# Optimization experiments

Hardware: AMD Instinct MI355X
Metric: run time of the kernel (lower is better)

## Reference

```python
import jax, jax.numpy as jnp
import numpy as np

N, F_IN, F_OUT, K = 4096, 32, 32, 2
NEG_SLOPE = 0.2
MASK_VAL = -9e15


def _sparse_mat(kv, km, density=0.01):
    vals = jax.random.normal(kv, (N, N), dtype=jnp.float32)
    mask = jax.random.uniform(km, (N, N)) < density
    return vals * mask


def setup_inputs() -> dict:
    key = jax.random.key(0)
    ks = jax.random.split(key, 12)
    x = jax.random.normal(ks[0], (N, F_IN), dtype=jnp.float32)
    Ld = _sparse_mat(ks[1], ks[2])
    Lu = _sparse_mat(ks[3], ks[4])
    P = jax.random.normal(ks[5], (N, N), dtype=jnp.float32) / np.sqrt(N)
    W1 = jax.random.normal(ks[6], (K, F_IN, F_OUT), dtype=jnp.float32) * 0.1
    W2 = jax.random.normal(ks[7], (K, F_IN, F_OUT), dtype=jnp.float32) * 0.1
    W0 = jax.random.normal(ks[8], (F_IN, F_OUT), dtype=jnp.float32) * 0.1
    att1 = jax.random.normal(ks[9], (2 * F_OUT * K, 1), dtype=jnp.float32) * 0.1
    att2 = jax.random.normal(ks[10], (2 * F_OUT * K, 1), dtype=jnp.float32) * 0.1
    return {"x": x, "Ld": Ld, "Lu": Lu, "P": P, "W1": W1, "W2": W2,
            "W0": W0, "att1": att1, "att2": att2}


def _branch(x, L, W, att):
    # W: [K, F_in, F_out]; precompute x @ W[k] for all k -> [K, N, F_out]
    Kk, _, Fo = W.shape
    xw = jnp.einsum('nf,kfo->kno', x, W)
    # torch.cat([x@W[k]], dim=1) == transpose+reshape of xw
    xcat = jnp.transpose(xw, (1, 0, 2)).reshape(x.shape[0], Kk * Fo)
    d = Fo * Kk
    e = xcat @ att[:d] + (xcat @ att[d:]).T            # [N, N]
    e = jax.nn.leaky_relu(e, negative_slope=NEG_SLOPE)
    e = jnp.where(L != 0, e, MASK_VAL)
    alpha = jax.nn.softmax(e, axis=1)                   # row softmax, no dropout (eval)
    z = alpha @ xw[0]
    a = alpha
    for k in range(1, Kk):
        a = a @ L
        z = z + a @ xw[k]
    return z


def reference(x, Ld, Lu, P, W1, W2, W0, att1, att2):
    z1 = _branch(x, Ld, W1, att1)
    z2 = _branch(x, Lu, W2, att2)
    x0 = P @ (x @ W0)
    return z1 + z2 + x0
```

## Files before the change

### kernel.cpp

```cpp
#include <hip/hip_runtime.h>
#include <hip/hip_bf16.h>

#define NN 4096
#define CAP 128
#define KS 8
#define PGB 512

typedef __attribute__((ext_vector_type(8))) short bf16x8;
typedef __attribute__((ext_vector_type(4))) float f32x4;

__device__ __forceinline__ float lrelu(float v) { return v >= 0.f ? v : 0.2f * v; }

__device__ __forceinline__ ushort f2bu(float f) {
    unsigned u = __float_as_uint(f);
    return (ushort)((u + 0x7FFFu + ((u >> 16) & 1u)) >> 16);
}

__global__ __launch_bounds__(256) void k_prep(
    const float* __restrict__ x,
    const float* __restrict__ W1, const float* __restrict__ W2,
    const float* __restrict__ W0,
    const float* __restrict__ att1, const float* __restrict__ att2,
    float* __restrict__ xwA1, float* __restrict__ xwB1,
    float* __restrict__ xwA2, float* __restrict__ xwB2,
    float* __restrict__ a1, float* __restrict__ b1,
    float* __restrict__ a2, float* __restrict__ b2,
    __hip_bfloat16* __restrict__ Bt)
{
    __shared__ float wl[5120];
    __shared__ float xs[256];
    const int t = threadIdx.x;
    for (int i = t; i < 2048; i += 256) { wl[i] = W1[i]; wl[2048 + i] = W2[i]; }
    for (int i = t; i < 1024; i += 256) wl[4096 + i] = W0[i];
    const int rowBase = blockIdx.x * 8;
    xs[t] = x[rowBase * 32 + t];
    __syncthreads();

    const int o = t & 31, r = t >> 5;
    const int row = rowBase + r;
    const float* xr = &xs[r * 32];
    float vA1 = 0.f, vB1 = 0.f, vA2 = 0.f, vB2 = 0.f, v0 = 0.f;
#pragma unroll
    for (int f = 0; f < 32; ++f) {
        const float xv = xr[f];
        vA1 += xv * wl[f * 32 + o];
        vB1 += xv * wl[1024 + f * 32 + o];
        vA2 += xv * wl[2048 + f * 32 + o];
        vB2 += xv * wl[3072 + f * 32 + o];
        v0  += xv * wl[4096 + f * 32 + o];
    }
    xwA1[row * 32 + o] = vA1;
    xwB1[row * 32 + o] = vB1;
    xwA2[row * 32 + o] = vA2;
    xwB2[row * 32 + o] = vB2;
    ((ushort*)Bt)[(size_t)o * NN + row] = f2bu(v0);

    float pa1 = vA1 * att1[o]      + vB1 * att1[32 + o];
    float pb1 = vA1 * att1[64 + o] + vB1 * att1[96 + o];
    float pa2 = vA2 * att2[o]      + vB2 * att2[32 + o];
    float pb2 = vA2 * att2[64 + o] + vB2 * att2[96 + o];
#pragma unroll
    for (int m = 1; m <= 16; m <<= 1) {
        pa1 += __shfl_xor(pa1, m); pb1 += __shfl_xor(pb1, m);
        pa2 += __shfl_xor(pa2, m); pb2 += __shfl_xor(pb2, m);
    }
    if (o == 0) { a1[row] = pa1; b1[row] = pb1; a2[row] = pa2; b2[row] = pb2; }
}

__global__ __launch_bounds__(256) void k_fused(
    const float* __restrict__ Ld, const float* __restrict__ Lu,
    const float* __restrict__ xwB1, const float* __restrict__ xwB2,
    const float* __restrict__ xwA1, const float* __restrict__ xwA2,
    const float* __restrict__ a1, const float* __restrict__ b1,
    const float* __restrict__ a2, const float* __restrict__ b2,
    int2* __restrict__ csrv, int* __restrict__ cntArr,
    float* __restrict__ u1, float* __restrict__ u2,
    const float* __restrict__ P, const ushort* __restrict__ Bt,
    float* __restrict__ partial)
{
    __shared__ int   sidx[CAP];
    __shared__ float sval[CAP];
    __shared__ int   wcnt[16];
    __shared__ float red[256];
    __shared__ float rpart[8];

    const int bid = blockIdx.x;
    const int t = threadIdx.x;
    const int lane = t & 63, w = t >> 6;

    if (bid < PGB) {
        const int gw = bid * 4 + w;
        const int mt = gw & 255;
        const int ks = gw >> 8;
        const int m0 = mt * 16;
        const int r  = lane & 15;
        const int kq = lane >> 4;

        const float*  pa  = P  + (size_t)(m0 + r) * NN + ks * 512 + kq * 8;
        const ushort* pb0 = Bt + (size_t)r        * NN + ks * 512 + kq * 8;
        const ushort* pb1 = Bt + (size_t)(16 + r) * NN + ks * 512 + kq * 8;

        f32x4 acc0 = {0.f, 0.f, 0.f, 0.f};
        f32x4 acc1 = {0.f, 0.f, 0.f, 0.f};

#pragma unroll 4
        for (int kk = 0; kk < 16; ++kk) {
            const float4 a0 = *(const float4*)(pa + kk * 32);
            const float4 a1v = *(const float4*)(pa + kk * 32 + 4);
            const bf16x8 b0 = *(const bf16x8*)(pb0 + kk * 32);
            const bf16x8 b1v = *(const bf16x8*)(pb1 + kk * 32);
            bf16x8 a;
            a[0] = (short)f2bu(a0.x); a[1] = (short)f2bu(a0.y);
            a[2] = (short)f2bu(a0.z); a[3] = (short)f2bu(a0.w);
            a[4] = (short)f2bu(a1v.x); a[5] = (short)f2bu(a1v.y);
            a[6] = (short)f2bu(a1v.z); a[7] = (short)f2bu(a1v.w);
            acc0 = __builtin_amdgcn_mfma_f32_16x16x32_bf16(a, b0, acc0, 0, 0, 0);
            acc1 = __builtin_amdgcn_mfma_f32_16x16x32_bf16(a, b1v, acc1, 0, 0, 0);
        }

        float* out = partial + ((size_t)ks * NN + m0 + kq * 4) * 32;
#pragma unroll
        for (int rr = 0; rr < 4; ++rr) {
            out[rr * 32 + r]      = acc0[rr];
            out[rr * 32 + 16 + r] = acc1[rr];
        }
        return;
    }

    const int sb  = bid - PGB;
    const int br  = sb >> 12;
    const int row = sb & (NN - 1);
    const float* L   = br ? Lu : Ld;
    const float* xwB = br ? xwB2 : xwB1;
    const float* xwA = br ? xwA2 : xwA1;
    const float* aA  = br ? a2 : a1;
    const float* bA  = br ? b2 : b1;
    int2* csrB = csrv + ((size_t)br * NN + row) * CAP;
    float* u   = br ? u2 : u1;

    const float4* L4 = (const float4*)(L + (size_t)row * NN);
    float4 v[4];
#pragma unroll
    for (int it = 0; it < 4; ++it) v[it] = L4[it * 256 + t];

    const unsigned long long lt = (1ull << lane) - 1ull;

    unsigned long long M0[4], M1[4], M2[4], M3[4];
    int tots[4];
#pragma unroll
    for (int it = 0; it < 4; ++it) {
        M0[it] = __ballot(v[it].x != 0.f);
        M1[it] = __ballot(v[it].y != 0.f);
        M2[it] = __ballot(v[it].z != 0.f);
        M3[it] = __ballot(v[it].w != 0.f);
        tots[it] = __popcll(M0[it]) + __popcll(M1[it]) + __popcll(M2[it]) + __popcll(M3[it]);
    }
    if (lane == 0) {
        int4 tv; tv.x = tots[0]; tv.y = tots[1]; tv.z = tots[2]; tv.w = tots[3];
        *(int4*)&wcnt[w * 4] = tv;
    }
    __syncthreads();

    const int4 ca = *(const int4*)&wcnt[0];
    const int4 cb = *(const int4*)&wcnt[4];
    const int4 cc = *(const int4*)&wcnt[8];
    const int4 cd = *(const int4*)&wcnt[12];
    const int cs[16] = {ca.x, ca.y, ca.z, ca.w, cb.x, cb.y, cb.z, cb.w,
                        cc.x, cc.y, cc.z, cc.w, cd.x, cd.y, cd.z, cd.w};
    int total = 0;
#pragma unroll
    for (int k2 = 0; k2 < 16; ++k2) total += cs[k2];
    int base = 0;
#pragma unroll
    for (int k2 = 0; k2 < 16; ++k2) base += (k2 < (w << 2)) ? cs[k2] : 0;

    const int cnt  = min(total, CAP);
    const int cp16 = min((cnt + 15) & ~15, CAP);

#pragma unroll
    for (int it = 0; it < 4; ++it) {
        const float vx = v[it].x, vy = v[it].y, vz = v[it].z, vw = v[it].w;
        const int p0 = __popcll(M0[it]), p1 = __popcll(M1[it]), p2 = __popcll(M2[it]);
        const int c0 = (it * 256 + t) * 4;
        int s;
        s = base + __popcll(M0[it] & lt);
        if (vx != 0.f && s < CAP) { sidx[s] = c0;     sval[s] = vx; }
        s = base + p0 + __popcll(M1[it] & lt);
        if (vy != 0.f && s < CAP) { sidx[s] = c0 + 1; sval[s] = vy; }
        s = base + p0 + p1 + __popcll(M2[it] & lt);
        if (vz != 0.f && s < CAP) { sidx[s] = c0 + 2; sval[s] = vz; }
        s = base + p0 + p1 + p2 + __popcll(M3[it] & lt);
        if (vw != 0.f && s < CAP) { sidx[s] = c0 + 3; sval[s] = vw; }
        base += p0 + p1 + p2 + __popcll(M3[it]);
    }
    if (t >= cnt && t < cp16) { sidx[t] = 0; sval[t] = 0.f; }
    __syncthreads();

    const float ai = aA[row];
    const int myidx = (t < cp16) ? sidx[t] : 0;
    const float e = (t < cnt) ? lrelu(ai + bA[myidx]) : -1e30f;
    float m = e;
#pragma unroll
    for (int mm = 1; mm <= 32; mm <<= 1) m = fmaxf(m, __shfl_xor(m, mm));
    if (lane == 0) rpart[w] = m;
    __syncthreads();
    m = fmaxf(fmaxf(rpart[0], rpart[1]), fmaxf(rpart[2], rpart[3]));
    const float wgt = (t < cnt) ? __expf(e - m) : 0.f;
    float ss = wgt;
#pragma unroll
    for (int mm = 1; mm <= 32; mm <<= 1) ss += __shfl_xor(ss, mm);
    if (lane == 0) rpart[4 + w] = ss;
    __syncthreads();
    const float ssum = rpart[4] + rpart[5] + rpart[6] + rpart[7];
    const float inv = (cnt > 0) ? 1.f / ssum : 0.f;
    if (t < cp16) { int2 eo; eo.x = myidx; eo.y = __float_as_int(wgt * inv); csrB[t] = eo; }
    if (t == 0) cntArr[br * NN + row] = cnt;

    const int o = t & 31, g = t >> 5;
    float acc = 0.f;
    const int nPair = cp16 >> 4;
    if (nPair > 0) {
        float vA0 = sval[g],      vA1 = sval[g + 8];
        float xA0 = xwB[(size_t)sidx[g] * 32 + o];
        float xA1 = xwB[(size_t)sidx[g + 8] * 32 + o];
        for (int j = 1; j < nPair; ++j) {
            const int sB = g + 16 * j;
            const float vB0 = sval[sB],  vB1 = sval[sB + 8];
            const float xB0 = xwB[(size_t)sidx[sB] * 32 + o];
            const float xB1 = xwB[(size_t)sidx[sB + 8] * 32 + o];
            acc += vA0 * xA0 + vA1 * xA1;
            vA0 = vB0; xA0 = xB0; vA1 = vB1; xA1 = xB1;
        }
        acc += vA0 * xA0 + vA1 * xA1;
    }
    red[t] = acc;
    __syncthreads();
    if (t < 32) {
        float tot2 = 0.f;
#pragma unroll
        for (int g2 = 0; g2 < 8; ++g2) tot2 += red[g2 * 32 + t];
        u[(size_t)row * 32 + t] = tot2 + xwA[(size_t)row * 32 + t];
    }
}

__global__ __launch_bounds__(256) void k_accum(
    const int2* __restrict__ csrv, const int* __restrict__ cntArr,
    const float* __restrict__ u1, const float* __restrict__ u2,
    const float* __restrict__ partial, float* __restrict__ outp)
{
    __shared__ int2 sle[4][2 * CAP];
    const int w = threadIdx.x >> 6, lane = threadIdx.x & 63;
    const int row = blockIdx.x * 4 + w;
    const int o = lane & 31, g = lane >> 5;
    int2* se = sle[w];
    float total = 0.f;

    int cp[2];
#pragma unroll
    for (int br = 0; br < 2; ++br) {
        const int cnt = cntArr[br * NN + row];
        cp[br] = min((cnt + 15) & ~15, CAP);
        const int2* ci = csrv + ((size_t)br * NN + row) * CAP;
        if (lane < cp[br])      se[br * CAP + lane]      = ci[lane];
        if (lane + 64 < cp[br]) se[br * CAP + lane + 64] = ci[lane + 64];
    }

#pragma unroll
    for (int br = 0; br < 2; ++br) {
        const float* U = br ? u2 : u1;
        float acc = 0.f;
        const int nb = cp[br] >> 3;
        for (int j = 0; j < nb; ++j) {
            float wv[4], uv[4];
#pragma unroll
            for (int q = 0; q < 4; ++q) {
                const int2 e = se[br * CAP + 8 * j + 2 * q + g];
                wv[q] = __int_as_float(e.y);
                uv[q] = U[(size_t)e.x * 32 + o];
            }
#pragma unroll
            for (int q = 0; q < 4; ++q) acc += wv[q] * uv[q];
        }
        acc += __shfl_xor(acc, 32);
        total += acc;
    }

    if (lane < 32) {
#pragma unroll
        for (int p = 0; p < KS; ++p)
            total += partial[(size_t)p * NN * 32 + (size_t)row * 32 + o];
        outp[(size_t)row * 32 + o] = total;
    }
}

extern "C" void kernel_launch(void* const* d_in, const int* in_sizes, int n_in,
                              void* d_out, int out_size, void* d_ws, size_t ws_size,
                              hipStream_t stream) {
    (void)in_sizes; (void)n_in; (void)out_size; (void)ws_size;
    const float* x    = (const float*)d_in[0];
    const float* Ld   = (const float*)d_in[1];
    const float* Lu   = (const float*)d_in[2];
    const float* P    = (const float*)d_in[3];
    const float* W1   = (const float*)d_in[4];
    const float* W2   = (const float*)d_in[5];
    const float* W0   = (const float*)d_in[6];
    const float* att1 = (const float*)d_in[7];
    const float* att2 = (const float*)d_in[8];

    float* ws = (float*)d_ws;
    float* xwA1 = ws;
    float* xwB1 = ws + 131072;
    float* xwA2 = ws + 262144;
    float* xwB2 = ws + 393216;
    float* u1   = ws + 524288;
    float* u2   = ws + 655360;
    float* a1   = ws + 786432;
    float* b1   = ws + 790528;
    float* a2   = ws + 794624;
    float* b2   = ws + 798720;
    float* partial = ws + 802816;
    __hip_bfloat16* Bt = (__hip_bfloat16*)(ws + 1851392);
    int2* csrv = (int2*)(ws + 1916928);
    int*  cnt  = (int*)(ws + 4014080);

    k_prep<<<512, 256, 0, stream>>>(x, W1, W2, W0, att1, att2,
                                    xwA1, xwB1, xwA2, xwB2, a1, b1, a2, b2, Bt);
    k_fused<<<PGB + 2 * NN, 256, 0, stream>>>(Ld, Lu, xwB1, xwB2, xwA1, xwA2,
                                              a1, b1, a2, b2, csrv, cnt, u1, u2,
                                              P, (const ushort*)Bt, partial);
    k_accum<<<NN / 4, 256, 0, stream>>>(csrv, cnt, u1, u2, partial,
                                        (float*)d_out);
}
```

Baseline: 224.2 us.

## Merge fused and accumulate kernels into persistent kernel with grid barrier

```diff
diff --git a/kernel.cpp b/kernel.cpp
--- a/kernel.cpp
+++ b/kernel.cpp
@@ -25,8 +25,10 @@
     float* __restrict__ xwA2, float* __restrict__ xwB2,
     float* __restrict__ a1, float* __restrict__ b1,
     float* __restrict__ a2, float* __restrict__ b2,
-    __hip_bfloat16* __restrict__ Bt)
+    __hip_bfloat16* __restrict__ Bt, unsigned* __restrict__ ctr)
 {
+    if (blockIdx.x == 0 && threadIdx.x < 2) ctr[threadIdx.x] = 0u;
+
     __shared__ float wl[5120];
     __shared__ float xs[256];
     const int t = threadIdx.x;
@@ -67,7 +69,7 @@
     if (o == 0) { a1[row] = pa1; b1[row] = pb1; a2[row] = pa2; b2[row] = pb2; }
 }
 
-__global__ __launch_bounds__(256) void k_fused(
+__global__ __launch_bounds__(256) void k_mega(
     const float* __restrict__ Ld, const float* __restrict__ Lu,
     const float* __restrict__ xwB1, const float* __restrict__ xwB2,
     const float* __restrict__ xwA1, const float* __restrict__ xwA2,
@@ -76,205 +78,205 @@
     int2* __restrict__ csrv, int* __restrict__ cntArr,
     float* __restrict__ u1, float* __restrict__ u2,
     const float* __restrict__ P, const ushort* __restrict__ Bt,
-    float* __restrict__ partial)
+    float* __restrict__ partial, float* __restrict__ outp,
+    unsigned* __restrict__ ctr, int B)
 {
-    __shared__ int   sidx[CAP];
-    __shared__ float sval[CAP];
-    __shared__ int   wcnt[16];
-    __shared__ float red[256];
-    __shared__ float rpart[8];
+    __shared__ union {
+        struct {
+            int   sidx[CAP];
+            float sval[CAP];
+            int   wcnt[16];
+            float red[256];
+            float rpart[8];
+        } s;
+        float sacc[4][32];
+    } sh;
 
     const int bid = blockIdx.x;
     const int t = threadIdx.x;
     const int lane = t & 63, w = t >> 6;
 
-    if (bid < PGB) {
-        const int gw = bid * 4 + w;
-        const int mt = gw & 255;
-        const int ks = gw >> 8;
-        const int m0 = mt * 16;
-        const int r  = lane & 15;
-        const int kq = lane >> 4;
-
-        const float*  pa  = P  + (size_t)(m0 + r) * NN + ks * 512 + kq * 8;
-        const ushort* pb0 = Bt + (size_t)r        * NN + ks * 512 + kq * 8;
-        const ushort* pb1 = Bt + (size_t)(16 + r) * NN + ks * 512 + kq * 8;
-
-        f32x4 acc0 = {0.f, 0.f, 0.f, 0.f};
-        f32x4 acc1 = {0.f, 0.f, 0.f, 0.f};
+    for (int vb = bid; vb < PGB + 2 * NN; vb += B) {
+        if (vb < PGB) {
+            const int gw = vb * 4 + w;
+            const int mt = gw & 255;
+            const int ks = gw >> 8;
+            const int m0 = mt * 16;
+            const int r  = lane & 15;
+            const int kq = lane >> 4;
+
+            const float*  pa  = P  + (size_t)(m0 + r) * NN + ks * 512 + kq * 8;
+            const ushort* pb0 = Bt + (size_t)r        * NN + ks * 512 + kq * 8;
+            const ushort* pb1 = Bt + (size_t)(16 + r) * NN + ks * 512 + kq * 8;
+
+            f32x4 acc0 = {0.f, 0.f, 0.f, 0.f};
+            f32x4 acc1 = {0.f, 0.f, 0.f, 0.f};
 
 #pragma unroll 4
-        for (int kk = 0; kk < 16; ++kk) {
-            const float4 a0 = *(const float4*)(pa + kk * 32);
-            const float4 a1v = *(const float4*)(pa + kk * 32 + 4);
-            const bf16x8 b0 = *(const bf16x8*)(pb0 + kk * 32);
-            const bf16x8 b1v = *(const bf16x8*)(pb1 + kk * 32);
-            bf16x8 a;
-            a[0] = (short)f2bu(a0.x); a[1] = (short)f2bu(a0.y);
-            a[2] = (short)f2bu(a0.z); a[3] = (short)f2bu(a0.w);
-            a[4] = (short)f2bu(a1v.x); a[5] = (short)f2bu(a1v.y);
-            a[6] = (short)f2bu(a1v.z); a[7] = (short)f2bu(a1v.w);
-            acc0 = __builtin_amdgcn_mfma_f32_16x16x32_bf16(a, b0, acc0, 0, 0, 0);
-            acc1 = __builtin_amdgcn_mfma_f32_16x16x32_bf16(a, b1v, acc1, 0, 0, 0);
-        }
-
-        float* out = partial + ((size_t)ks * NN + m0 + kq * 4) * 32;
-#pragma unroll
-        for (int rr = 0; rr < 4; ++rr) {
-            out[rr * 32 + r]      = acc0[rr];
-            out[rr * 32 + 16 + r] = acc1[rr];
-        }
-        return;
-    }
-
-    const int sb  = bid - PGB;
-    const int br  = sb >> 12;
-    const int row = sb & (NN - 1);
-    const float* L   = br ? Lu : Ld;
-    const float* xwB = br ? xwB2 : xwB1;
-    const float* xwA = br ? xwA2 : xwA1;
-    const float* aA  = br ? a2 : a1;
-    const float* bA  = br ? b2 : b1;
-    int2* csrB = csrv + ((size_t)br * NN + row) * CAP;
-    float* u   = br ? u2 : u1;
-
-    const float4* L4 = (const float4*)(L + (size_t)row * NN);
-    float4 v[4];
-#pragma unroll
-    for (int it = 0; it < 4; ++it) v[it] = L4[it * 256 + t];
-
-    const unsigned long long lt = (1ull << lane) - 1ull;
-
-    unsigned long long M0[4], M1[4], M2[4], M3[4];
-    int tots[4];
-#pragma unroll
-    for (int it = 0; it < 4; ++it) {
-        M0[it] = __ballot(v[it].x != 0.f);
-        M1[it] = __ballot(v[it].y != 0.f);
-        M2[it] = __ballot(v[it].z != 0.f);
-        M3[it] = __ballot(v[it].w != 0.f);
-        tots[it] = __popcll(M0[it]) + __popcll(M1[it]) + __popcll(M2[it]) + __popcll(M3[it]);
-    }
-    if (lane == 0) {
-        int4 tv; tv.x = tots[0]; tv.y = tots[1]; tv.z = tots[2]; tv.w = tots[3];
-        *(int4*)&wcnt[w * 4] = tv;
-    }
+            for (int kk = 0; kk < 16; ++kk) {
+                const float4 a0  = *(const float4*)(pa + kk * 32);
+                const float4 a1v = *(const float4*)(pa + kk * 32 + 4);
+                const bf16x8 b0  = *(const bf16x8*)(pb0 + kk * 32);
+                const bf16x8 b1v = *(const bf16x8*)(pb1 + kk * 32);
+                bf16x8 a;
+                a[0] = (short)f2bu(a0.x);  a[1] = (short)f2bu(a0.y);
+                a[2] = (short)f2bu(a0.z);  a[3] = (short)f2bu(a0.w);
+                a[4] = (short)f2bu(a1v.x); a[5] = (short)f2bu(a1v.y);
+                a[6] = (short)f2bu(a1v.z); a[7] = (short)f2bu(a1v.w);
+                acc0 = __builtin_amdgcn_mfma_f32_16x16x32_bf16(a, b0, acc0, 0, 0, 0);
+                acc1 = __builtin_amdgcn_mfma_f32_16x16x32_bf16(a, b1v, acc1, 0, 0, 0);
+            }
+
+            float* out = partial + ((size_t)ks * NN + m0 + kq * 4) * 32;
+#pragma unroll
+            for (int rr = 0; rr < 4; ++rr) {
+                out[rr * 32 + r]      = acc0[rr];
+                out[rr * 32 + 16 + r] = acc1[rr];
+            }
+            continue;
+        }
+
+        const int sb  = vb - PGB;
+        const int br  = sb >> 12;
+        const int row = sb & (NN - 1);
+        const float* L   = br ? Lu : Ld;
+        const float* xwB = br ? xwB2 : xwB1;
+        const float* xwA = br ? xwA2 : xwA1;
+        const float* aA  = br ? a2 : a1;
+        const float* bA  = br ? b2 : b1;
+        int2* csrB = csrv + ((size_t)br * NN + row) * CAP;
+        float* u   = br ? u2 : u1;
+
+        const float4* L4 = (const float4*)(L + (size_t)row * NN);
+        float4 v[4];
+#pragma unroll
+        for (int it = 0; it < 4; ++it) v[it] = L4[it * 256 + t];
+
+        const unsigned long long lt = (1ull << lane) - 1ull;
+
+        unsigned long long M0[4], M1[4], M2[4], M3[4];
+        int tots[4];
+#pragma unroll
+        for (int it = 0; it < 4; ++it) {
+            M0[it] = __ballot(v[it].x != 0.f);
+            M1[it] = __ballot(v[it].y != 0.f);
+            M2[it] = __ballot(v[it].z != 0.f);
+            M3[it] = __ballot(v[it].w != 0.f);
+            tots[it] = __popcll(M0[it]) + __popcll(M1[it]) + __popcll(M2[it]) + __popcll(M3[it]);
+        }
+        if (lane == 0) {
+            int4 tv; tv.x = tots[0]; tv.y = tots[1]; tv.z = tots[2]; tv.w = tots[3];
+            *(int4*)&sh.s.wcnt[w * 4] = tv;
+        }
+        __syncthreads();
+
+        const int4 ca = *(const int4*)&sh.s.wcnt[0];
+        const int4 cb = *(const int4*)&sh.s.wcnt[4];
+        const int4 cc = *(const int4*)&sh.s.wcnt[8];
+        const int4 cd = *(const int4*)&sh.s.wcnt[12];
+        const int cs[16] = {ca.x, ca.y, ca.z, ca.w, cb.x, cb.y, cb.z, cb.w,
+                            cc.x, cc.y, cc.z, cc.w, cd.x, cd.y, cd.z, cd.w};
+        int total = 0;
+#pragma unroll
+        for (int k2 = 0; k2 < 16; ++k2) total += cs[k2];
+        int base = 0;
+#pragma unroll
+        for (int k2 = 0; k2 < 16; ++k2) base += (k2 < (w << 2)) ? cs[k2] : 0;
+
+        const int cnt  = min(total, CAP);
+        const int cp16 = min((cnt + 15) & ~15, CAP);
+
+#pragma unroll
+        for (int it = 0; it < 4; ++it) {
+            const float vx = v[it].x, vy = v[it].y, vz = v[it].z, vw = v[it].w;
+            const int p0 = __popcll(M0[it]), p1 = __popcll(M1[it]), p2 = __popcll(M2[it]);
+            const int c0 = (it * 256 + t) * 4;
+            int s;
+            s = base + __popcll(M0[it] & lt);
+            if (vx != 0.f && s < CAP) { sh.s.sidx[s] = c0;     sh.s.sval[s] = vx; }
+            s = base + p0 + __popcll(M1[it] & lt);
+            if (vy != 0.f && s < CAP) { sh.s.sidx[s] = c0 + 1; sh.s.sval[s] = vy; }
+            s = base + p0 + p1 + __popcll(M2[it] & lt);
+            if (vz != 0.f && s < CAP) { sh.s.sidx[s] = c0 + 2; sh.s.sval[s] = vz; }
+            s = base + p0 + p1 + p2 + __popcll(M3[it] & lt);
+            if (vw != 0.f && s < CAP) { sh.s.sidx[s] = c0 + 3; sh.s.sval[s] = vw; }
+            base += p0 + p1 + p2 + __popcll(M3[it]);
+        }
+        if (t >= cnt && t < cp16) { sh.s.sidx[t] = 0; sh.s.sval[t] = 0.f; }
+        __syncthreads();
+
+        const float ai = aA[row];
+        const int myidx = (t < cp16) ? sh.s.sidx[t] : 0;
+        const float e = (t < cnt) ? lrelu(ai + bA[myidx]) : -1e30f;
+        float m = e;
+#pragma unroll
+        for (int mm = 1; mm <= 32; mm <<= 1) m = fmaxf(m, __shfl_xor(m, mm));
+        if (lane == 0) sh.s.rpart[w] = m;
+        __syncthreads();
+        m = fmaxf(fmaxf(sh.s.rpart[0], sh.s.rpart[1]), fmaxf(sh.s.rpart[2], sh.s.rpart[3]));
+        const float wgt = (t < cnt) ? __expf(e - m) : 0.f;
+        float ss = wgt;
+#pragma unroll
+        for (int mm = 1; mm <= 32; mm <<= 1) ss += __shfl_xor(ss, mm);
+        if (lane == 0) sh.s.rpart[4 + w] = ss;
+        __syncthreads();
+        const float ssum = sh.s.rpart[4] + sh.s.rpart[5] + sh.s.rpart[6] + sh.s.rpart[7];
+        const float inv = (cnt > 0) ? 1.f / ssum : 0.f;
+        if (t < cp16) { int2 eo; eo.x = myidx; eo.y = __float_as_int(wgt * inv); csrB[t] = eo; }
+        if (t == 0) cntArr[br * NN + row] = cnt;
+
+        const int o = t & 31, g = t >> 5;
+        float acc = 0.f;
+        const int nPair = cp16 >> 4;
+        if (nPair > 0) {
+            float vA0 = sh.s.sval[g],      vA1 = sh.s.sval[g + 8];
+            float xA0 = xwB[(size_t)sh.s.sidx[g] * 32 + o];
+            float xA1 = xwB[(size_t)sh.s.sidx[g + 8] * 32 + o];
+            for (int j = 1; j < nPair; ++j) {
+                const int sB = g + 16 * j;
+                const float vB0 = sh.s.sval[sB],  vB1 = sh.s.sval[sB + 8];
+                const float xB0 = xwB[(size_t)sh.s.sidx[sB] * 32 + o];
+                const float xB1 = xwB[(size_t)sh.s.sidx[sB + 8] * 32 + o];
+                acc += vA0 * xA0 + vA1 * xA1;
+                vA0 = vB0; xA0 = xB0; vA1 = vB1; xA1 = xB1;
+            }
+            acc += vA0 * xA0 + vA1 * xA1;
+        }
+        sh.s.red[t] = acc;
+        __syncthreads();
+        if (t < 32) {
+            float tot2 = 0.f;
+#pragma unroll
+            for (int g2 = 0; g2 < 8; ++g2) tot2 += sh.s.red[g2 * 32 + t];
+            u[(size_t)row * 32 + t] = tot2 + xwA[(size_t)row * 32 + t];
+        }
+    }
+
     __syncthreads();
-
-    const int4 ca = *(const int4*)&wcnt[0];
-    const int4 cb = *(const int4*)&wcnt[4];
-    const int4 cc = *(const int4*)&wcnt[8];
-    const int4 cd = *(const int4*)&wcnt[12];
-    const int cs[16] = {ca.x, ca.y, ca.z, ca.w, cb.x, cb.y, cb.z, cb.w,
-                        cc.x, cc.y, cc.z, cc.w, cd.x, cd.y, cd.z, cd.w};
-    int total = 0;
-#pragma unroll
-    for (int k2 = 0; k2 < 16; ++k2) total += cs[k2];
-    int base = 0;
-#pragma unroll
-    for (int k2 = 0; k2 < 16; ++k2) base += (k2 < (w << 2)) ? cs[k2] : 0;
-
-    const int cnt  = min(total, CAP);
-    const int cp16 = min((cnt + 15) & ~15, CAP);
-
-#pragma unroll
-    for (int it = 0; it < 4; ++it) {
-        const float vx = v[it].x, vy = v[it].y, vz = v[it].z, vw = v[it].w;
-        const int p0 = __popcll(M0[it]), p1 = __popcll(M1[it]), p2 = __popcll(M2[it]);
-        const int c0 = (it * 256 + t) * 4;
-        int s;
-        s = base + __popcll(M0[it] & lt);
-        if (vx != 0.f && s < CAP) { sidx[s] = c0;     sval[s] = vx; }
-        s = base + p0 + __popcll(M1[it] & lt);
-        if (vy != 0.f && s < CAP) { sidx[s] = c0 + 1; sval[s] = vy; }
-        s = base + p0 + p1 + __popcll(M2[it] & lt);
-        if (vz != 0.f && s < CAP) { sidx[s] = c0 + 2; sval[s] = vz; }
-        s = base + p0 + p1 + p2 + __popcll(M3[it] & lt);
-        if (vw != 0.f && s < CAP) { sidx[s] = c0 + 3; sval[s] = vw; }
-        base += p0 + p1 + p2 + __popcll(M3[it]);
-    }
-    if (t >= cnt && t < cp16) { sidx[t] = 0; sval[t] = 0.f; }
+    if (t == 0) {
+        __threadfence();
+        atomicAdd(&ctr[0], 1u);
+        while (__hip_atomic_load(&ctr[0], __ATOMIC_ACQUIRE,
+                                 __HIP_MEMORY_SCOPE_AGENT) < (unsigned)B)
+            __builtin_amdgcn_s_sleep(8);
+    }
     __syncthreads();
 
-    const float ai = aA[row];
-    const int myidx = (t < cp16) ? sidx[t] : 0;
-    const float e = (t < cnt) ? lrelu(ai + bA[myidx]) : -1e30f;
-    float m = e;
-#pragma unroll
-    for (int mm = 1; mm <= 32; mm <<= 1) m = fmaxf(m, __shfl_xor(m, mm));
-    if (lane == 0) rpart[w] = m;
-    __syncthreads();
-    m = fmaxf(fmaxf(rpart[0], rpart[1]), fmaxf(rpart[2], rpart[3]));
-    const float wgt = (t < cnt) ? __expf(e - m) : 0.f;
-    float ss = wgt;
-#pragma unroll
-    for (int mm = 1; mm <= 32; mm <<= 1) ss += __shfl_xor(ss, mm);
-    if (lane == 0) rpart[4 + w] = ss;
-    __syncthreads();
-    const float ssum = rpart[4] + rpart[5] + rpart[6] + rpart[7];
-    const float inv = (cnt > 0) ? 1.f / ssum : 0.f;
-    if (t < cp16) { int2 eo; eo.x = myidx; eo.y = __float_as_int(wgt * inv); csrB[t] = eo; }
-    if (t == 0) cntArr[br * NN + row] = cnt;
-
-    const int o = t & 31, g = t >> 5;
-    float acc = 0.f;
-    const int nPair = cp16 >> 4;
-    if (nPair > 0) {
-        float vA0 = sval[g],      vA1 = sval[g + 8];
-        float xA0 = xwB[(size_t)sidx[g] * 32 + o];
-        float xA1 = xwB[(size_t)sidx[g + 8] * 32 + o];
-        for (int j = 1; j < nPair; ++j) {
-            const int sB = g + 16 * j;
-            const float vB0 = sval[sB],  vB1 = sval[sB + 8];
-            const float xB0 = xwB[(size_t)sidx[sB] * 32 + o];
-            const float xB1 = xwB[(size_t)sidx[sB + 8] * 32 + o];
-            acc += vA0 * xA0 + vA1 * xA1;
-            vA0 = vB0; xA0 = xB0; vA1 = vB1; xA1 = xB1;
-        }
-        acc += vA0 * xA0 + vA1 * xA1;
-    }
-    red[t] = acc;
-    __syncthreads();
-    if (t < 32) {
-        float tot2 = 0.f;
-#pragma unroll
-        for (int g2 = 0; g2 < 8; ++g2) tot2 += red[g2 * 32 + t];
-        u[(size_t)row * 32 + t] = tot2 + xwA[(size_t)row * 32 + t];
-    }
-}
-
-__global__ __launch_bounds__(256) void k_accum(
-    const int2* __restrict__ csrv, const int* __restrict__ cntArr,
-    const float* __restrict__ u1, const float* __restrict__ u2,
-    const float* __restrict__ partial, float* __restrict__ outp)
-{
-    __shared__ int2 sle[4][2 * CAP];
-    const int w = threadIdx.x >> 6, lane = threadIdx.x & 63;
-    const int row = blockIdx.x * 4 + w;
-    const int o = lane & 31, g = lane >> 5;
-    int2* se = sle[w];
-    float total = 0.f;
-
-    int cp[2];
-#pragma unroll
-    for (int br = 0; br < 2; ++br) {
+    for (int vb = bid; vb < NN / 2; vb += B) {
+        const int row = vb * 2 + (w >> 1);
+        const int br  = w & 1;
+        const float* U = br ? u2 : u1;
         const int cnt = cntArr[br * NN + row];
-        cp[br] = min((cnt + 15) & ~15, CAP);
+        const int cp  = min((cnt + 15) & ~15, CAP);
         const int2* ci = csrv + ((size_t)br * NN + row) * CAP;
-        if (lane < cp[br])      se[br * CAP + lane]      = ci[lane];
-        if (lane + 64 < cp[br]) se[br * CAP + lane + 64] = ci[lane + 64];
-    }
-
-#pragma unroll
-    for (int br = 0; br < 2; ++br) {
-        const float* U = br ? u2 : u1;
+        const int o = lane & 31, g = lane >> 5;
         float acc = 0.f;
-        const int nb = cp[br] >> 3;
+        const int nb = cp >> 3;
         for (int j = 0; j < nb; ++j) {
             float wv[4], uv[4];
 #pragma unroll
             for (int q = 0; q < 4; ++q) {
-                const int2 e = se[br * CAP + 8 * j + 2 * q + g];
+                const int2 e = ci[8 * j + 2 * q + g];
                 wv[q] = __int_as_float(e.y);
                 uv[q] = U[(size_t)e.x * 32 + o];
             }
@@ -282,14 +284,16 @@
             for (int q = 0; q < 4; ++q) acc += wv[q] * uv[q];
         }
         acc += __shfl_xor(acc, 32);
-        total += acc;
-    }
-
-    if (lane < 32) {
-#pragma unroll
-        for (int p = 0; p < KS; ++p)
-            total += partial[(size_t)p * NN * 32 + (size_t)row * 32 + o];
-        outp[(size_t)row * 32 + o] = total;
+        if (lane < 32) sh.sacc[w][o] = acc;
+        __syncthreads();
+        if ((w & 1) == 0 && lane < 32) {
+            float total = sh.sacc[w][o] + sh.sacc[w + 1][o];
+#pragma unroll
+            for (int p = 0; p < KS; ++p)
+                total += partial[(size_t)p * NN * 32 + (size_t)row * 32 + o];
+            outp[(size_t)row * 32 + o] = total;
+        }
+        __syncthreads();
     }
 }
 
@@ -322,12 +326,24 @@
     __hip_bfloat16* Bt = (__hip_bfloat16*)(ws + 1851392);
     int2* csrv = (int2*)(ws + 1916928);
     int*  cnt  = (int*)(ws + 4014080);
+    unsigned* ctr = (unsigned*)(ws + 4022272);
+
+    static int occ_cached = -1;
+    if (occ_cached < 0) {
+        int occ = 0;
+        if (hipOccupancyMaxActiveBlocksPerMultiprocessor(&occ, k_mega, 256, 0)
+                != hipSuccess || occ <= 0)
+            occ = 4;
+        occ_cached = occ;
+    }
+    int B = occ_cached * 256;
+    if (B > 2048) B = 2048;
 
     k_prep<<<512, 256, 0, stream>>>(x, W1, W2, W0, att1, att2,
-                                    xwA1, xwB1, xwA2, xwB2, a1, b1, a2, b2, Bt);
-    k_fused<<<PGB + 2 * NN, 256, 0, stream>>>(Ld, Lu, xwB1, xwB2, xwA1, xwA2,
-                                              a1, b1, a2, b2, csrv, cnt, u1, u2,
-                                              P, (const ushort*)Bt, partial);
-    k_accum<<<NN / 4, 256, 0, stream>>>(csrv, cnt, u1, u2, partial,
-                                        (float*)d_out);
+                                    xwA1, xwB1, xwA2, xwB2, a1, b1, a2, b2,
+                                    (__hip_bfloat16*)Bt, ctr);
+    k_mega<<<B, 256, 0, stream>>>(Ld, Lu, xwB1, xwB2, xwA1, xwA2,
+                                  a1, b1, a2, b2, csrv, cnt, u1, u2,
+                                  P, (const ushort*)Bt, partial,
+                                  (float*)d_out, ctr, B);
 }
```

New measurement: 322.4 us. +43.8%, slower.

## Shrink fused kernel blocks to 128 threads and simplify row compaction

Applied to the files above, without the earlier changes.

```diff
diff --git a/kernel.cpp b/kernel.cpp
--- a/kernel.cpp
+++ b/kernel.cpp
@@ -4,7 +4,7 @@
 #define NN 4096
 #define CAP 128
 #define KS 8
-#define PGB 512
+#define PGB 1024
 
 typedef __attribute__((ext_vector_type(8))) short bf16x8;
 typedef __attribute__((ext_vector_type(4))) float f32x4;
@@ -67,7 +67,7 @@
     if (o == 0) { a1[row] = pa1; b1[row] = pb1; a2[row] = pa2; b2[row] = pb2; }
 }
 
-__global__ __launch_bounds__(256) void k_fused(
+__global__ __launch_bounds__(128) void k_fused(
     const float* __restrict__ Ld, const float* __restrict__ Lu,
     const float* __restrict__ xwB1, const float* __restrict__ xwB2,
     const float* __restrict__ xwA1, const float* __restrict__ xwA2,
@@ -80,16 +80,16 @@
 {
     __shared__ int   sidx[CAP];
     __shared__ float sval[CAP];
-    __shared__ int   wcnt[16];
-    __shared__ float red[256];
-    __shared__ float rpart[8];
+    __shared__ float red[128];
+    __shared__ int   wtot[2];
+    __shared__ float rpart[4];
 
     const int bid = blockIdx.x;
     const int t = threadIdx.x;
     const int lane = t & 63, w = t >> 6;
 
     if (bid < PGB) {
-        const int gw = bid * 4 + w;
+        const int gw = bid * 2 + w;
         const int mt = gw & 255;
         const int ks = gw >> 8;
         const int m0 = mt * 16;
@@ -105,13 +105,13 @@
 
 #pragma unroll 4
         for (int kk = 0; kk < 16; ++kk) {
-            const float4 a0 = *(const float4*)(pa + kk * 32);
+            const float4 a0  = *(const float4*)(pa + kk * 32);
             const float4 a1v = *(const float4*)(pa + kk * 32 + 4);
-            const bf16x8 b0 = *(const bf16x8*)(pb0 + kk * 32);
+            const bf16x8 b0  = *(const bf16x8*)(pb0 + kk * 32);
             const bf16x8 b1v = *(const bf16x8*)(pb1 + kk * 32);
             bf16x8 a;
-            a[0] = (short)f2bu(a0.x); a[1] = (short)f2bu(a0.y);
-            a[2] = (short)f2bu(a0.z); a[3] = (short)f2bu(a0.w);
+            a[0] = (short)f2bu(a0.x);  a[1] = (short)f2bu(a0.y);
+            a[2] = (short)f2bu(a0.z);  a[3] = (short)f2bu(a0.w);
             a[4] = (short)f2bu(a1v.x); a[5] = (short)f2bu(a1v.y);
             a[6] = (short)f2bu(a1v.z); a[7] = (short)f2bu(a1v.w);
             acc0 = __builtin_amdgcn_mfma_f32_16x16x32_bf16(a, b0, acc0, 0, 0, 0);
@@ -139,59 +139,48 @@
     float* u   = br ? u2 : u1;
 
     const float4* L4 = (const float4*)(L + (size_t)row * NN);
-    float4 v[4];
-#pragma unroll
-    for (int it = 0; it < 4; ++it) v[it] = L4[it * 256 + t];
+    float4 v[8];
+#pragma unroll
+    for (int j = 0; j < 8; ++j) v[j] = L4[j * 128 + t];
 
     const unsigned long long lt = (1ull << lane) - 1ull;
 
-    unsigned long long M0[4], M1[4], M2[4], M3[4];
-    int tots[4];
-#pragma unroll
-    for (int it = 0; it < 4; ++it) {
-        M0[it] = __ballot(v[it].x != 0.f);
-        M1[it] = __ballot(v[it].y != 0.f);
-        M2[it] = __ballot(v[it].z != 0.f);
-        M3[it] = __ballot(v[it].w != 0.f);
-        tots[it] = __popcll(M0[it]) + __popcll(M1[it]) + __popcll(M2[it]) + __popcll(M3[it]);
-    }
-    if (lane == 0) {
-        int4 tv; tv.x = tots[0]; tv.y = tots[1]; tv.z = tots[2]; tv.w = tots[3];
-        *(int4*)&wcnt[w * 4] = tv;
-    }
-    __syncthreads();
-
-    const int4 ca = *(const int4*)&wcnt[0];
-    const int4 cb = *(const int4*)&wcnt[4];
-    const int4 cc = *(const int4*)&wcnt[8];
-    const int4 cd = *(const int4*)&wcnt[12];
-    const int cs[16] = {ca.x, ca.y, ca.z, ca.w, cb.x, cb.y, cb.z, cb.w,
-                        cc.x, cc.y, cc.z, cc.w, cd.x, cd.y, cd.z, cd.w};
-    int total = 0;
-#pragma unroll
-    for (int k2 = 0; k2 < 16; ++k2) total += cs[k2];
-    int base = 0;
-#pragma unroll
-    for (int k2 = 0; k2 < 16; ++k2) base += (k2 < (w << 2)) ? cs[k2] : 0;
-
+    int tw = 0;
+#pragma unroll
+    for (int j = 0; j < 8; ++j) {
+        tw += __popcll(__ballot(v[j].x != 0.f));
+        tw += __popcll(__ballot(v[j].y != 0.f));
+        tw += __popcll(__ballot(v[j].z != 0.f));
+        tw += __popcll(__ballot(v[j].w != 0.f));
+    }
+    if (lane == 0) wtot[w] = tw;
+    __syncthreads();
+
+    const int t0 = wtot[0];
+    const int total = t0 + wtot[1];
     const int cnt  = min(total, CAP);
     const int cp16 = min((cnt + 15) & ~15, CAP);
-
-#pragma unroll
-    for (int it = 0; it < 4; ++it) {
-        const float vx = v[it].x, vy = v[it].y, vz = v[it].z, vw = v[it].w;
-        const int p0 = __popcll(M0[it]), p1 = __popcll(M1[it]), p2 = __popcll(M2[it]);
-        const int c0 = (it * 256 + t) * 4;
+    int base = w ? t0 : 0;
+
+#pragma unroll
+    for (int j = 0; j < 8; ++j) {
+        const float vx = v[j].x, vy = v[j].y, vz = v[j].z, vw = v[j].w;
+        const unsigned long long m0 = __ballot(vx != 0.f);
+        const unsigned long long m1 = __ballot(vy != 0.f);
+        const unsigned long long m2 = __ballot(vz != 0.f);
+        const unsigned long long m3 = __ballot(vw != 0.f);
+        const int p0 = __popcll(m0), p1 = __popcll(m1), p2 = __popcll(m2);
+        const int c0 = (j * 128 + t) * 4;
         int s;
-        s = base + __popcll(M0[it] & lt);
+        s = base + __popcll(m0 & lt);
         if (vx != 0.f && s < CAP) { sidx[s] = c0;     sval[s] = vx; }
-        s = base + p0 + __popcll(M1[it] & lt);
+        s = base + p0 + __popcll(m1 & lt);
         if (vy != 0.f && s < CAP) { sidx[s] = c0 + 1; sval[s] = vy; }
-        s = base + p0 + p1 + __popcll(M2[it] & lt);
+        s = base + p0 + p1 + __popcll(m2 & lt);
         if (vz != 0.f && s < CAP) { sidx[s] = c0 + 2; sval[s] = vz; }
-        s = base + p0 + p1 + p2 + __popcll(M3[it] & lt);
+        s = base + p0 + p1 + p2 + __popcll(m3 & lt);
         if (vw != 0.f && s < CAP) { sidx[s] = c0 + 3; sval[s] = vw; }
-        base += p0 + p1 + p2 + __popcll(M3[it]);
+        base += p0 + p1 + p2 + __popcll(m3);
     }
     if (t >= cnt && t < cp16) { sidx[t] = 0; sval[t] = 0.f; }
     __syncthreads();
@@ -204,41 +193,36 @@
     for (int mm = 1; mm <= 32; mm <<= 1) m = fmaxf(m, __shfl_xor(m, mm));
     if (lane == 0) rpart[w] = m;
     __syncthreads();
-    m = fmaxf(fmaxf(rpart[0], rpart[1]), fmaxf(rpart[2], rpart[3]));
+    m = fmaxf(rpart[0], rpart[1]);
     const float wgt = (t < cnt) ? __expf(e - m) : 0.f;
     float ss = wgt;
 #pragma unroll
     for (int mm = 1; mm <= 32; mm <<= 1) ss += __shfl_xor(ss, mm);
-    if (lane == 0) rpart[4 + w] = ss;
-    __syncthreads();
-    const float ssum = rpart[4] + rpart[5] + rpart[6] + rpart[7];
+    if (lane == 0) rpart[2 + w] = ss;
+    __syncthreads();
+    const float ssum = rpart[2] + rpart[3];
     const float inv = (cnt > 0) ? 1.f / ssum : 0.f;
     if (t < cp16) { int2 eo; eo.x = myidx; eo.y = __float_as_int(wgt * inv); csrB[t] = eo; }
     if (t == 0) cntArr[br * NN + row] = cnt;
 
     const int o = t & 31, g = t >> 5;
     float acc = 0.f;
-    const int nPair = cp16 >> 4;
-    if (nPair > 0) {
-        float vA0 = sval[g],      vA1 = sval[g + 8];
-        float xA0 = xwB[(size_t)sidx[g] * 32 + o];
-        float xA1 = xwB[(size_t)sidx[g + 8] * 32 + o];
-        for (int j = 1; j < nPair; ++j) {
-            const int sB = g + 16 * j;
-            const float vB0 = sval[sB],  vB1 = sval[sB + 8];
-            const float xB0 = xwB[(size_t)sidx[sB] * 32 + o];
-            const float xB1 = xwB[(size_t)sidx[sB + 8] * 32 + o];
-            acc += vA0 * xA0 + vA1 * xA1;
-            vA0 = vB0; xA0 = xB0; vA1 = vB1; xA1 = xB1;
+    for (int s0 = 0; s0 < cp16; s0 += 16) {
+        float vv[4], uu[4];
+#pragma unroll
+        for (int q = 0; q < 4; ++q) {
+            const int sl = s0 + 4 * q + g;
+            const int ix = sidx[sl];
+            vv[q] = sval[sl];
+            uu[q] = xwB[(size_t)ix * 32 + o];
         }
-        acc += vA0 * xA0 + vA1 * xA1;
+#pragma unroll
+        for (int q = 0; q < 4; ++q) acc += vv[q] * uu[q];
     }
     red[t] = acc;
     __syncthreads();
     if (t < 32) {
-        float tot2 = 0.f;
-#pragma unroll
-        for (int g2 = 0; g2 < 8; ++g2) tot2 += red[g2 * 32 + t];
+        const float tot2 = red[t] + red[32 + t] + red[64 + t] + red[96 + t];
         u[(size_t)row * 32 + t] = tot2 + xwA[(size_t)row * 32 + t];
     }
 }
@@ -325,7 +309,7 @@
 
     k_prep<<<512, 256, 0, stream>>>(x, W1, W2, W0, att1, att2,
                                     xwA1, xwB1, xwA2, xwB2, a1, b1, a2, b2, Bt);
-    k_fused<<<PGB + 2 * NN, 256, 0, stream>>>(Ld, Lu, xwB1, xwB2, xwA1, xwA2,
+    k_fused<<<PGB + 2 * NN, 128, 0, stream>>>(Ld, Lu, xwB1, xwB2, xwA1, xwA2,
                                               a1, b1, a2, b2, csrv, cnt, u1, u2,
                                               P, (const ushort*)Bt, partial);
     k_accum<<<NN / 4, 256, 0, stream>>>(csrv, cnt, u1, u2, partial,
```

Result: no change. 221.9 us (-1.0%).
